# Optimization experiments

Measured on AMD Instinct MI355X. Metric: run time of the kernel, lower is better.

Reference implementation:

```python
import jax, jax.numpy as jnp
import numpy as np
import math

N_HEADS = 8
TANH_CLIP = 10.0
TEMP = 1.0


def setup_inputs() -> dict:
    key = jax.random.key(0)
    ks = jax.random.split(key, 8)
    B, N, D = 256, 2048, 128
    node_embeddings = jax.random.normal(ks[0], (B, N, D), dtype=jnp.float32)
    W_node = jax.random.normal(ks[1], (D, 3 * D), dtype=jnp.float32) / math.sqrt(D)
    W_fixed = jax.random.normal(ks[2], (D, D), dtype=jnp.float32) / math.sqrt(D)
    W_step = jax.random.normal(ks[3], (2 * D, D), dtype=jnp.float32) / math.sqrt(2 * D)
    W_out = jax.random.normal(ks[4], (D, D), dtype=jnp.float32) / math.sqrt(D)
    first_idx = jax.random.randint(ks[5], (B,), 0, N, dtype=jnp.int32)
    last_idx = jax.random.randint(ks[6], (B,), 0, N, dtype=jnp.int32)
    mask = jax.random.bernoulli(ks[7], 0.5, (B, N))
    mask = mask.at[:, 0].set(False)  # guarantee at least one feasible node per row
    return {"node_embeddings": node_embeddings, "W_node": W_node, "W_fixed": W_fixed,
            "W_step": W_step, "W_out": W_out, "first_idx": first_idx,
            "last_idx": last_idx, "mask": mask}


def reference(node_embeddings, W_node, W_fixed, W_step, W_out, first_idx, last_idx, mask):
    B, N, D = node_embeddings.shape
    H = N_HEADS
    hd = D // H  # key_dim = val_dim = embed_dim / n_heads
    neg_inf = -jnp.inf

    # --- _precompute ---
    graph_embed = node_embeddings.mean(axis=1)                # [B, D]
    fixed_context = graph_embed @ W_fixed                     # [B, D]
    proj = node_embeddings @ W_node                           # [B, N, 3D]
    gK, gV, logit_K = jnp.split(proj, 3, axis=-1)             # each [B, N, D]
    gK = gK.reshape(B, N, H, hd).transpose(2, 0, 1, 3)        # [H, B, N, hd]
    gV = gV.reshape(B, N, H, hd).transpose(2, 0, 1, 3)        # [H, B, N, hd]

    # --- step context: cat(first node emb, last node emb) ---
    first_emb = jnp.take_along_axis(node_embeddings, first_idx[:, None, None].astype(jnp.int32), axis=1)[:, 0]  # [B, D]
    last_emb = jnp.take_along_axis(node_embeddings, last_idx[:, None, None].astype(jnp.int32), axis=1)[:, 0]
    step_ctx = jnp.concatenate([first_emb, last_emb], axis=-1)  # [B, 2D]
    query = fixed_context + step_ctx @ W_step                 # [B, D]

    # --- glimpse multi-head attention (n_query = 1, masked inner) ---
    Q = query.reshape(B, H, hd).transpose(1, 0, 2)            # [H, B, hd]
    compat = jnp.einsum('hbd,hbnd->hbn', Q, gK) / math.sqrt(hd)  # [H, B, N]
    compat = jnp.where(mask[None, :, :], neg_inf, compat)     # mask_inner=True
    attn = jax.nn.softmax(compat, axis=-1)
    heads = jnp.einsum('hbn,hbnd->hbd', attn, gV)             # [H, B, hd]
    glimpse = heads.transpose(1, 0, 2).reshape(B, D) @ W_out  # project_out, [B, D]

    # --- logits with tanh clipping and masking ---
    logits = jnp.einsum('bd,bnd->bn', glimpse, logit_K) / math.sqrt(D)  # [B, N]
    logits = jnp.tanh(logits) * TANH_CLIP
    logits = jnp.where(mask, neg_inf, logits)                 # mask_logits=True
    log_p = jax.nn.log_softmax(logits / TEMP, axis=-1)        # [B, N]
    return log_p
```

## Files before the change

kernel.cpp:

```cpp
#include <hip/hip_runtime.h>
#include <math.h>

#define B_ 256
#define N_ 2048
#define D_ 128

#define NEG_HUGE (-1.0e30f)

#define WSA_STRIDE 1040
#define WSA_SIZE (B_ * 8 * WSA_STRIDE)
#define WSB_OFF WSA_SIZE
#define WSB_SIZE (B_ * 8 * 2)
#define WSC_OFF (WSB_OFF + WSB_SIZE)
#define WSC_SIZE (B_ * D_)
#define WS_FLOATS (WSC_OFF + WSC_SIZE)

__device__ __forceinline__ float wave_max64(float v) {
#pragma unroll
  for (int off = 32; off > 0; off >>= 1) v = fmaxf(v, __shfl_xor(v, off, 64));
  return v;
}
__device__ __forceinline__ float wave_sum64(float v) {
#pragma unroll
  for (int off = 32; off > 0; off >>= 1) v += __shfl_xor(v, off, 64);
  return v;
}

__global__ void __launch_bounds__(128) k_partial(const float* __restrict__ emb,
                                                 float* __restrict__ buf) {
  const int b = blockIdx.x, s = blockIdx.y;
  const int t = threadIdx.x;
  const int f4 = t & 31, ng = t >> 5;
  const float4* base = (const float4*)(emb + (size_t)b * N_ * D_);
  float4 acc = make_float4(0.f, 0.f, 0.f, 0.f);
  int n = s * 256 + ng;
#pragma unroll 4
  for (int i = 0; i < 64; ++i, n += 4) {
    float4 v = base[(size_t)n * 32 + f4];
    acc.x += v.x; acc.y += v.y; acc.z += v.z; acc.w += v.w;
  }
  __shared__ float4 red[128];
  red[t] = acc;
  __syncthreads();
  if (ng == 0) {
    float4 a = red[f4], bb = red[32 + f4], c = red[64 + f4], d = red[96 + f4];
    float4 r = make_float4(a.x + bb.x + c.x + d.x, a.y + bb.y + c.y + d.y,
                           a.z + bb.z + c.z + d.z, a.w + bb.w + c.w + d.w);
    *((float4*)(buf + (size_t)b * N_ + s * 128) + f4) = r;
  }
}

__global__ void __launch_bounds__(128) k_query(const float* __restrict__ emb,
                                               const float* __restrict__ Wfix,
                                               const float* __restrict__ Wstep,
                                               const float* __restrict__ Wnode,
                                               const int* __restrict__ fidx,
                                               const int* __restrict__ lidx,
                                               float* __restrict__ buf) {
  const int b = blockIdx.x, t = threadIdx.x;
  __shared__ float ge[128], fe[128], le[128], q[128];
  float s = 0.f;
  const float* part = buf + (size_t)b * N_;
#pragma unroll
  for (int i = 0; i < 8; ++i) s += part[i * 128 + t];
  ge[t] = s * (1.0f / 2048.0f);
  const int fi = fidx[b], li = lidx[b];
  fe[t] = emb[(size_t)b * N_ * D_ + (size_t)fi * D_ + t];
  le[t] = emb[(size_t)b * N_ * D_ + (size_t)li * D_ + t];
  __syncthreads();
  float acc = 0.f;
  for (int k = 0; k < 128; ++k) acc = fmaf(ge[k], Wfix[k * 128 + t], acc);
  for (int k = 0; k < 128; ++k) acc = fmaf(fe[k], Wstep[k * 128 + t], acc);
  for (int k = 0; k < 128; ++k) acc = fmaf(le[k], Wstep[(128 + k) * 128 + t], acc);
  q[t] = acc;
  __syncthreads();
  const float* wrow = Wnode + (size_t)t * 384;
#pragma unroll
  for (int h = 0; h < 8; ++h) {
    float a = 0.f;
#pragma unroll
    for (int k = 0; k < 16; ++k) a = fmaf(q[h * 16 + k], wrow[h * 16 + k], a);
    buf[(size_t)b * N_ + 1024 + h * 128 + t] = a * 0.25f;
  }
}

__global__ void __launch_bounds__(256) k_attn_part(const float* __restrict__ emb,
                                                   const unsigned char* __restrict__ mask,
                                                   const float* __restrict__ buf,
                                                   float* __restrict__ wsA) {
  const int b = blockIdx.x, s = blockIdx.y;
  const int t = threadIdx.x;
  const int lane = t & 63;
  const int hb = t >> 6;
  const int h0 = hb, h1 = hb + 4;

  __shared__ __align__(16) float emb_lds[64][132];
  __shared__ __align__(16) float qh_s[8 * 128];
  __shared__ unsigned char mask_s[64];

  {
    const float* src = buf + (size_t)b * N_ + 1024;
    for (int i = t; i < 1024; i += 256) qh_s[i] = src[i];
  }

  float m0 = -INFINITY, m1 = -INFINITY, l0 = 0.f, l1 = 0.f;
  float w00 = 0.f, w01 = 0.f, w10 = 0.f, w11 = 0.f;
  const int d0 = lane, d1 = lane + 64;
  const float* embb = emb + (size_t)b * N_ * D_;
  const unsigned char* mrow = mask + (size_t)b * N_;

  __syncthreads();

  for (int tile = 0; tile < 4; ++tile) {
    const int n0 = s * 256 + tile * 64;
    {
      int gid = t;
#pragma unroll
      for (int i = 0; i < 8; ++i, gid += 256) {
        int r = gid >> 5, c4 = gid & 31;
        float4 v = *(const float4*)(embb + (size_t)(n0 + r) * D_ + c4 * 4);
        *(float4*)&emb_lds[r][c4 * 4] = v;
      }
      if (t < 64) mask_s[t] = mrow[n0 + t];
    }
    __syncthreads();

    float s0 = 0.f, s1 = 0.f;
    {
      const float* er = &emb_lds[lane][0];
      const float* q0r = &qh_s[h0 * 128];
      const float* q1r = &qh_s[h1 * 128];
#pragma unroll 8
      for (int k = 0; k < 32; ++k) {
        float4 e = *(const float4*)(er + 4 * k);
        float4 qa = *(const float4*)(q0r + 4 * k);
        float4 qb = *(const float4*)(q1r + 4 * k);
        s0 = fmaf(e.x, qa.x, fmaf(e.y, qa.y, fmaf(e.z, qa.z, fmaf(e.w, qa.w, s0))));
        s1 = fmaf(e.x, qb.x, fmaf(e.y, qb.y, fmaf(e.z, qb.z, fmaf(e.w, qb.w, s1))));
      }
    }
    const bool msk = mask_s[lane] != 0;
    if (msk) { s0 = -INFINITY; s1 = -INFINITY; }

    const float tm0 = wave_max64(s0), tm1 = wave_max64(s1);
    const float mn0 = fmaxf(m0, tm0), mn1 = fmaxf(m1, tm1);
    const float r0 = (mn0 == -INFINITY) ? 1.f : expf(m0 - mn0);
    const float r1 = (mn1 == -INFINITY) ? 1.f : expf(m1 - mn1);
    const float p0 = msk ? 0.f : expf(s0 - mn0);
    const float p1 = msk ? 0.f : expf(s1 - mn1);
    l0 = l0 * r0 + wave_sum64(p0);
    l1 = l1 * r1 + wave_sum64(p1);
    m0 = mn0; m1 = mn1;

    w00 *= r0; w01 *= r0; w10 *= r1; w11 *= r1;
#pragma unroll 4
    for (int n = 0; n < 64; ++n) {
      const float pa = __int_as_float(__builtin_amdgcn_readlane(__float_as_int(p0), n));
      const float pb = __int_as_float(__builtin_amdgcn_readlane(__float_as_int(p1), n));
      const float e0 = emb_lds[n][d0];
      const float e1 = emb_lds[n][d1];
      w00 = fmaf(pa, e0, w00); w01 = fmaf(pa, e1, w01);
      w10 = fmaf(pb, e0, w10); w11 = fmaf(pb, e1, w11);
    }
    __syncthreads();
  }

  float* dst = wsA + (size_t)(b * 8 + s) * WSA_STRIDE;
  dst[16 + h0 * 128 + d0] = w00;
  dst[16 + h0 * 128 + d1] = w01;
  dst[16 + h1 * 128 + d0] = w10;
  dst[16 + h1 * 128 + d1] = w11;
  if (lane == 0) {
    dst[h0] = m0; dst[8 + h0] = l0;
    dst[h1] = m1; dst[8 + h1] = l1;
  }
}

__global__ void __launch_bounds__(128) k_attn_comb(const float* __restrict__ Wnode,
                                                   const float* __restrict__ Wout,
                                                   const float* __restrict__ wsA,
                                                   float* __restrict__ wsC) {
  const int b = blockIdx.x, t = threadIdx.x;
  const float* base = wsA + (size_t)b * 8 * WSA_STRIDE;
  __shared__ float Ls[8], scale[8][8];
  __shared__ float wl[8 * 128], heads[128], glim[128];

  if (t < 8) {
    float M = -INFINITY;
#pragma unroll
    for (int s = 0; s < 8; ++s) M = fmaxf(M, base[s * WSA_STRIDE + t]);
    float L = 0.f;
#pragma unroll
    for (int s = 0; s < 8; ++s) {
      const float m = base[s * WSA_STRIDE + t];
      const float sc = (m == -INFINITY) ? 0.f : expf(m - M);
      scale[s][t] = sc;
      L = fmaf(base[s * WSA_STRIDE + 8 + t], sc, L);
    }
    Ls[t] = L;
  }
  __syncthreads();

#pragma unroll
  for (int h = 0; h < 8; ++h) {
    float acc = 0.f;
#pragma unroll
    for (int s = 0; s < 8; ++s)
      acc = fmaf(scale[s][h], base[s * WSA_STRIDE + 16 + h * 128 + t], acc);
    wl[h * 128 + t] = acc;
  }
  __syncthreads();

  {
    const int h = t >> 4, k = t & 15;
    float hv = 0.f;
    const float* wp = Wnode + 128 + h * 16 + k;
    for (int d = 0; d < 128; ++d) hv = fmaf(wl[h * 128 + d], wp[(size_t)d * 384], hv);
    heads[t] = hv / Ls[h];
  }
  __syncthreads();
  {
    float g = 0.f;
    for (int j = 0; j < 128; ++j) g = fmaf(heads[j], Wout[j * 128 + t], g);
    glim[t] = g;
  }
  __syncthreads();
  {
    float cv = 0.f;
    const float* wr = Wnode + (size_t)t * 384 + 256;
    for (int j = 0; j < 128; ++j) cv = fmaf(wr[j], glim[j], cv);
    wsC[(size_t)b * 128 + t] = cv * 0.08838834764831845f;
  }
}

__global__ void __launch_bounds__(256) k_logits_part(const float* __restrict__ emb,
                                                     const unsigned char* __restrict__ mask,
                                                     const float* __restrict__ wsC,
                                                     float* __restrict__ buf,
                                                     float* __restrict__ wsB) {
  const int b = blockIdx.x, s = blockIdx.y;
  const int t = threadIdx.x, lane = t & 63, w = t >> 6;
  __shared__ __align__(16) float emb_lds[64][132];
  __shared__ float part[4][64];
  const float* embb = emb + (size_t)b * N_ * D_;
  const unsigned char* mrow = mask + (size_t)b * N_;

  float4 cq[8];
  {
    const float4* c4 = (const float4*)(wsC + (size_t)b * 128);
#pragma unroll
    for (int j = 0; j < 8; ++j) cq[j] = c4[w * 8 + j];
  }

  float mr = NEG_HUGE, sr = 0.f;
  for (int tile = 0; tile < 4; ++tile) {
    const int n0 = s * 256 + tile * 64;
    {
      int gid = t;
#pragma unroll
      for (int i = 0; i < 8; ++i, gid += 256) {
        int r = gid >> 5, c4i = gid & 31;
        *(float4*)&emb_lds[r][c4i * 4] =
            *(const float4*)(embb + (size_t)(n0 + r) * D_ + c4i * 4);
      }
    }
    __syncthreads();

    const float* er = &emb_lds[lane][w * 32];
    float acc = 0.f;
#pragma unroll
    for (int j = 0; j < 8; ++j) {
      float4 e = *(const float4*)(er + 4 * j);
      acc = fmaf(e.x, cq[j].x, fmaf(e.y, cq[j].y, fmaf(e.z, cq[j].z, fmaf(e.w, cq[j].w, acc))));
    }
    part[w][lane] = acc;
    __syncthreads();

    const float v = part[0][lane] + part[1][lane] + part[2][lane] + part[3][lane];
    const bool msk = mrow[n0 + lane] != 0;
    const float val = msk ? NEG_HUGE : 10.f * tanhf(v);
    const float tm = wave_max64(val);
    const float mn = fmaxf(mr, tm);
    sr = sr * expf(mr - mn) + wave_sum64(msk ? 0.f : expf(val - mn));
    mr = mn;
    if (w == 0) buf[(size_t)b * N_ + n0 + lane] = val;
    __syncthreads();
  }
  if (t == 0) {
    wsB[(size_t)(b * 8 + s) * 2] = mr;
    wsB[(size_t)(b * 8 + s) * 2 + 1] = sr;
  }
}

__global__ void __launch_bounds__(256) k_norm(const float* __restrict__ wsB,
                                              float* __restrict__ buf) {
  const int b = blockIdx.x, t = threadIdx.x;
  __shared__ float LSs;
  if (t == 0) {
    float M = NEG_HUGE;
#pragma unroll
    for (int s = 0; s < 8; ++s) M = fmaxf(M, wsB[(size_t)(b * 8 + s) * 2]);
    float S = 0.f;
#pragma unroll
    for (int s = 0; s < 8; ++s) {
      const float m = wsB[(size_t)(b * 8 + s) * 2];
      S += wsB[(size_t)(b * 8 + s) * 2 + 1] * expf(m - M);
    }
    LSs = M + logf(S);
  }
  __syncthreads();
  const float LS = LSs;
#pragma unroll
  for (int i = 0; i < 8; ++i) {
    const size_t idx = (size_t)b * N_ + t + 256 * i;
    const float v = buf[idx];
    buf[idx] = (v <= -1.0e29f) ? NEG_HUGE : (v - LS);
  }
}

__global__ void __launch_bounds__(256) k_attn(const float* __restrict__ emb,
                                              const float* __restrict__ Wnode,
                                              const float* __restrict__ Wout,
                                              const unsigned char* __restrict__ mask,
                                              float* __restrict__ buf) {
  const int b = blockIdx.x;
  const int t = threadIdx.x;
  const int lane = t & 63;
  const int hb = t >> 6;
  const int h0 = hb, h1 = hb + 4;

  __shared__ __align__(16) float emb_lds[64][132];
  __shared__ __align__(16) float qh_s[8 * 128];
  __shared__ float heads_lds[128];
  __shared__ float glim_lds[128];
  __shared__ float l_lds[8];
  __shared__ unsigned char mask_s[64];

  {
    const float* src = buf + (size_t)b * N_ + 1024;
    for (int i = t; i < 1024; i += 256) qh_s[i] = src[i];
  }
  float m0 = -INFINITY, m1 = -INFINITY, l0 = 0.f, l1 = 0.f;
  float w00 = 0.f, w01 = 0.f, w10 = 0.f, w11 = 0.f;
  const int d0 = lane, d1 = lane + 64;
  const float* embb = emb + (size_t)b * N_ * D_;
  const unsigned char* mrow = mask + (size_t)b * N_;
  __syncthreads();
  for (int tile = 0; tile < N_ / 64; ++tile) {
    const int n0 = tile * 64;
    int gid = t;
#pragma unroll
    for (int i = 0; i < 8; ++i, gid += 256) {
      int r = gid >> 5, c4 = gid & 31;
      *(float4*)&emb_lds[r][c4 * 4] = *(const float4*)(embb + (size_t)(n0 + r) * D_ + c4 * 4);
    }
    if (t < 64) mask_s[t] = mrow[n0 + t];
    __syncthreads();
    float s0 = 0.f, s1 = 0.f;
    const float* er = &emb_lds[lane][0];
    const float* q0r = &qh_s[h0 * 128];
    const float* q1r = &qh_s[h1 * 128];
#pragma unroll 8
    for (int k = 0; k < 32; ++k) {
      float4 e = *(const float4*)(er + 4 * k);
      float4 qa = *(const float4*)(q0r + 4 * k);
      float4 qb = *(const float4*)(q1r + 4 * k);
      s0 = fmaf(e.x, qa.x, fmaf(e.y, qa.y, fmaf(e.z, qa.z, fmaf(e.w, qa.w, s0))));
      s1 = fmaf(e.x, qb.x, fmaf(e.y, qb.y, fmaf(e.z, qb.z, fmaf(e.w, qb.w, s1))));
    }
    const bool msk = mask_s[lane] != 0;
    if (msk) { s0 = -INFINITY; s1 = -INFINITY; }
    const float tm0 = wave_max64(s0), tm1 = wave_max64(s1);
    const float mn0 = fmaxf(m0, tm0), mn1 = fmaxf(m1, tm1);
    const float r0 = (mn0 == -INFINITY) ? 1.f : expf(m0 - mn0);
    const float r1 = (mn1 == -INFINITY) ? 1.f : expf(m1 - mn1);
    const float p0 = msk ? 0.f : expf(s0 - mn0);
    const float p1 = msk ? 0.f : expf(s1 - mn1);
    l0 = l0 * r0 + wave_sum64(p0);
    l1 = l1 * r1 + wave_sum64(p1);
    m0 = mn0; m1 = mn1;
    w00 *= r0; w01 *= r0; w10 *= r1; w11 *= r1;
#pragma unroll 4
    for (int n = 0; n < 64; ++n) {
      const float pa = __int_as_float(__builtin_amdgcn_readlane(__float_as_int(p0), n));
      const float pb = __int_as_float(__builtin_amdgcn_readlane(__float_as_int(p1), n));
      const float e0 = emb_lds[n][d0];
      const float e1 = emb_lds[n][d1];
      w00 = fmaf(pa, e0, w00); w01 = fmaf(pa, e1, w01);
      w10 = fmaf(pb, e0, w10); w11 = fmaf(pb, e1, w11);
    }
    __syncthreads();
  }
  float* wl = &emb_lds[0][0];
  wl[h0 * 128 + d0] = w00; wl[h0 * 128 + d1] = w01;
  wl[h1 * 128 + d0] = w10; wl[h1 * 128 + d1] = w11;
  if (lane == 0) { l_lds[h0] = l0; l_lds[h1] = l1; }
  __syncthreads();
  if (t < 128) {
    const int h = t >> 4, k = t & 15;
    float hv = 0.f;
    const float* wp = Wnode + 128 + h * 16 + k;
    for (int d = 0; d < 128; ++d) hv = fmaf(wl[h * 128 + d], wp[(size_t)d * 384], hv);
    heads_lds[h * 16 + k] = hv / l_lds[h];
  }
  __syncthreads();
  if (t < 128) {
    float g = 0.f;
    for (int j = 0; j < 128; ++j) g = fmaf(heads_lds[j], Wout[j * 128 + t], g);
    glim_lds[t] = g;
  }
  __syncthreads();
  if (t < 128) {
    float cv = 0.f;
    const float* wr = Wnode + (size_t)t * 384 + 256;
    for (int j = 0; j < 128; ++j) cv = fmaf(wr[j], glim_lds[j], cv);
    buf[(size_t)b * N_ + t] = cv * 0.08838834764831845f;
  }
}

__global__ void __launch_bounds__(256) k_logits(const float* __restrict__ emb,
                                                const unsigned char* __restrict__ mask,
                                                float* __restrict__ buf) {
  const int b = blockIdx.x, t = threadIdx.x;
  const int lane = t & 63, w = t >> 6;
  __shared__ float lg[N_];
  __shared__ float redmax[4], redsum[4];
  const float c0 = buf[(size_t)b * N_ + 2 * lane];
  const float c1 = buf[(size_t)b * N_ + 2 * lane + 1];
  const float2* ebase = (const float2*)(emb + (size_t)b * N_ * D_);
  for (int i = 0; i < 64; ++i) {
    const int n0 = w * 512 + i * 8;
    float sarr[8];
#pragma unroll
    for (int j = 0; j < 8; ++j) {
      float2 e = ebase[(size_t)(n0 + j) * 64 + lane];
      sarr[j] = fmaf(e.x, c0, e.y * c1);
    }
#pragma unroll
    for (int j = 0; j < 8; ++j) {
      const float v = wave_sum64(sarr[j]);
      if (lane == j) lg[n0 + j] = v;
    }
  }
  __syncthreads();
  const unsigned char* mrow = mask + (size_t)b * N_;
  float v[8];
  float vmax = NEG_HUGE;
#pragma unroll
  for (int i = 0; i < 8; ++i) {
    const int n = t + 256 * i;
    const float val = mrow[n] ? NEG_HUGE : 10.f * tanhf(lg[n]);
    v[i] = val;
    vmax = fmaxf(vmax, val);
  }
  vmax = wave_max64(vmax);
  if (lane == 0) redmax[w] = vmax;
  __syncthreads();
  const float M = fmaxf(fmaxf(redmax[0], redmax[1]), fmaxf(redmax[2], redmax[3]));
  float ss = 0.f;
#pragma unroll
  for (int i = 0; i < 8; ++i) ss += expf(v[i] - M);
  ss = wave_sum64(ss);
  if (lane == 0) redsum[w] = ss;
  __syncthreads();
  const float S = redsum[0] + redsum[1] + redsum[2] + redsum[3];
  const float LS = M + logf(S);
#pragma unroll
  for (int i = 0; i < 8; ++i) {
    const int n = t + 256 * i;
    buf[(size_t)b * N_ + n] = mrow[n] ? NEG_HUGE : (v[i] - LS);
  }
}

extern "C" void kernel_launch(void* const* d_in, const int* in_sizes, int n_in,
                              void* d_out, int out_size, void* d_ws, size_t ws_size,
                              hipStream_t stream) {
  (void)in_sizes; (void)n_in; (void)out_size;
  const float* emb = (const float*)d_in[0];
  const float* Wnode = (const float*)d_in[1];
  const float* Wfix = (const float*)d_in[2];
  const float* Wstep = (const float*)d_in[3];
  const float* Wout = (const float*)d_in[4];
  const int* fidx = (const int*)d_in[5];
  const int* lidx = (const int*)d_in[6];
  const unsigned char* mask = (const unsigned char*)d_in[7];
  float* buf = (float*)d_out;

  k_partial<<<dim3(B_, 8), 128, 0, stream>>>(emb, buf);
  k_query<<<B_, 128, 0, stream>>>(emb, Wfix, Wstep, Wnode, fidx, lidx, buf);

  if (ws_size >= (size_t)WS_FLOATS * sizeof(float)) {
    float* ws = (float*)d_ws;
    k_attn_part<<<dim3(B_, 8), 256, 0, stream>>>(emb, mask, buf, ws);
    k_attn_comb<<<B_, 128, 0, stream>>>(Wnode, Wout, ws, ws + WSC_OFF);
    k_logits_part<<<dim3(B_, 8), 256, 0, stream>>>(emb, mask, ws + WSC_OFF, buf, ws + WSB_OFF);
    k_norm<<<B_, 256, 0, stream>>>(ws + WSB_OFF, buf);
  } else {
    k_attn<<<B_, 256, 0, stream>>>(emb, Wnode, Wout, mask, buf);
    k_logits<<<B_, 256, 0, stream>>>(emb, mask, buf);
  }
}
```

Before: 199.8 us.

## Use bf16 MFMA for attention scores and weighted sums in partial attention

Rewrites the split-N attention kernel so the query-key scores and the probability-weighted embedding sums run on 16x16x32 bf16 MFMA instructions instead of scalar FP32 FMAs. Embedding tiles are converted to bf16 and stored in LDS in both row and transposed layouts, with the online softmax reduced across waves through shared memory. The fallback single-kernel path and the workspace-size check are removed. This trades FP32 precision for bf16 in the attention step and adds extra LDS transposes and barriers, while the kernel is likely still dominated by streaming the embeddings from memory.

```diff
diff --git a/kernel.cpp b/kernel.cpp
--- a/kernel.cpp
+++ b/kernel.cpp
@@ -12,8 +12,10 @@
 #define WSB_OFF WSA_SIZE
 #define WSB_SIZE (B_ * 8 * 2)
 #define WSC_OFF (WSB_OFF + WSB_SIZE)
-#define WSC_SIZE (B_ * D_)
-#define WS_FLOATS (WSC_OFF + WSC_SIZE)
+
+typedef __attribute__((ext_vector_type(8))) short bf16x8;
+typedef __attribute__((ext_vector_type(4))) float f32x4;
+typedef __attribute__((ext_vector_type(4))) unsigned short u16x4;
 
 __device__ __forceinline__ float wave_max64(float v) {
 #pragma unroll
@@ -24,6 +26,11 @@
 #pragma unroll
   for (int off = 32; off > 0; off >>= 1) v += __shfl_xor(v, off, 64);
   return v;
+}
+__device__ __forceinline__ unsigned short bf16rne(float f) {
+  unsigned u = __float_as_uint(f);
+  u += 0x7FFFu + ((u >> 16) & 1u);
+  return (unsigned short)(u >> 16);
 }
 
 __global__ void __launch_bounds__(128) k_partial(const float* __restrict__ emb,
@@ -84,96 +91,142 @@
   }
 }
 
-__global__ void __launch_bounds__(256) k_attn_part(const float* __restrict__ emb,
-                                                   const unsigned char* __restrict__ mask,
-                                                   const float* __restrict__ buf,
-                                                   float* __restrict__ wsA) {
-  const int b = blockIdx.x, s = blockIdx.y;
-  const int t = threadIdx.x;
-  const int lane = t & 63;
-  const int hb = t >> 6;
-  const int h0 = hb, h1 = hb + 4;
-
-  __shared__ __align__(16) float emb_lds[64][132];
-  __shared__ __align__(16) float qh_s[8 * 128];
+__global__ void __launch_bounds__(256) k_attn_m(const float* __restrict__ emb,
+                                                const unsigned char* __restrict__ mask,
+                                                const float* __restrict__ buf,
+                                                float* __restrict__ wsA) {
+  const int b = blockIdx.x, s = blockIdx.y, t = threadIdx.x;
+  const int lane = t & 63, w = t >> 6;
+  const int lg = lane >> 4, lc = lane & 15;
+
+  __shared__ __align__(16) unsigned short eR[64][136];
+  __shared__ __align__(16) unsigned short eC[128][72];
+  __shared__ __align__(16) unsigned short pT[16][72];
+  __shared__ float red0[4][16];
+  __shared__ float red1[4][16];
+  __shared__ float resc_s[16];
   __shared__ unsigned char mask_s[64];
 
-  {
-    const float* src = buf + (size_t)b * N_ + 1024;
-    for (int i = t; i < 1024; i += 256) qh_s[i] = src[i];
-  }
-
-  float m0 = -INFINITY, m1 = -INFINITY, l0 = 0.f, l1 = 0.f;
-  float w00 = 0.f, w01 = 0.f, w10 = 0.f, w11 = 0.f;
-  const int d0 = lane, d1 = lane + 64;
-  const float* embb = emb + (size_t)b * N_ * D_;
-  const unsigned char* mrow = mask + (size_t)b * N_;
-
-  __syncthreads();
+  bf16x8 bq[4];
+#pragma unroll
+  for (int ks = 0; ks < 4; ++ks)
+#pragma unroll
+    for (int j = 0; j < 8; ++j) bq[ks][j] = 0;
+  if (lc < 8) {
+    const float* qrow = buf + (size_t)b * N_ + 1024 + lc * 128;
+#pragma unroll
+    for (int ks = 0; ks < 4; ++ks)
+#pragma unroll
+      for (int j = 0; j < 8; ++j)
+        bq[ks][j] = (short)bf16rne(qrow[32 * ks + 8 * lg + j]);
+  }
+
+  float m_run = -INFINITY, l_run = 0.f;
+  f32x4 wacc0 = {0.f, 0.f, 0.f, 0.f}, wacc1 = {0.f, 0.f, 0.f, 0.f};
+  const float* embb = emb + ((size_t)b * N_ + s * 256) * D_;
+  const unsigned char* mrow = mask + (size_t)b * N_ + s * 256;
 
   for (int tile = 0; tile < 4; ++tile) {
-    const int n0 = s * 256 + tile * 64;
     {
-      int gid = t;
-#pragma unroll
-      for (int i = 0; i < 8; ++i, gid += 256) {
-        int r = gid >> 5, c4 = gid & 31;
-        float4 v = *(const float4*)(embb + (size_t)(n0 + r) * D_ + c4 * 4);
-        *(float4*)&emb_lds[r][c4 * 4] = v;
+      const float* src = embb + (size_t)tile * 64 * D_;
+#pragma unroll
+      for (int i = 0; i < 4; ++i) {
+        const int gid = t + 256 * i;
+        const int n = gid >> 4, d0 = (gid & 15) * 8;
+        const float4 v0 = *(const float4*)(src + (size_t)n * D_ + d0);
+        const float4 v1 = *(const float4*)(src + (size_t)n * D_ + d0 + 4);
+        bf16x8 ev;
+        ev[0] = (short)bf16rne(v0.x); ev[1] = (short)bf16rne(v0.y);
+        ev[2] = (short)bf16rne(v0.z); ev[3] = (short)bf16rne(v0.w);
+        ev[4] = (short)bf16rne(v1.x); ev[5] = (short)bf16rne(v1.y);
+        ev[6] = (short)bf16rne(v1.z); ev[7] = (short)bf16rne(v1.w);
+        *(bf16x8*)&eR[n][d0] = ev;
       }
-      if (t < 64) mask_s[t] = mrow[n0 + t];
-    }
-    __syncthreads();
-
-    float s0 = 0.f, s1 = 0.f;
+      if (t < 64) mask_s[t] = mrow[tile * 64 + t];
+    }
+    __syncthreads();
+
     {
-      const float* er = &emb_lds[lane][0];
-      const float* q0r = &qh_s[h0 * 128];
-      const float* q1r = &qh_s[h1 * 128];
-#pragma unroll 8
-      for (int k = 0; k < 32; ++k) {
-        float4 e = *(const float4*)(er + 4 * k);
-        float4 qa = *(const float4*)(q0r + 4 * k);
-        float4 qb = *(const float4*)(q1r + 4 * k);
-        s0 = fmaf(e.x, qa.x, fmaf(e.y, qa.y, fmaf(e.z, qa.z, fmaf(e.w, qa.w, s0))));
-        s1 = fmaf(e.x, qb.x, fmaf(e.y, qb.y, fmaf(e.z, qb.z, fmaf(e.w, qb.w, s1))));
+      const int d = t >> 1, n0 = (t & 1) * 32;
+#pragma unroll
+      for (int jb = 0; jb < 4; ++jb) {
+        bf16x8 cv;
+#pragma unroll
+        for (int i = 0; i < 8; ++i) cv[i] = (short)eR[n0 + 8 * jb + i][d];
+        *(bf16x8*)&eC[d][n0 + 8 * jb] = cv;
       }
     }
-    const bool msk = mask_s[lane] != 0;
-    if (msk) { s0 = -INFINITY; s1 = -INFINITY; }
-
-    const float tm0 = wave_max64(s0), tm1 = wave_max64(s1);
-    const float mn0 = fmaxf(m0, tm0), mn1 = fmaxf(m1, tm1);
-    const float r0 = (mn0 == -INFINITY) ? 1.f : expf(m0 - mn0);
-    const float r1 = (mn1 == -INFINITY) ? 1.f : expf(m1 - mn1);
-    const float p0 = msk ? 0.f : expf(s0 - mn0);
-    const float p1 = msk ? 0.f : expf(s1 - mn1);
-    l0 = l0 * r0 + wave_sum64(p0);
-    l1 = l1 * r1 + wave_sum64(p1);
-    m0 = mn0; m1 = mn1;
-
-    w00 *= r0; w01 *= r0; w10 *= r1; w11 *= r1;
-#pragma unroll 4
-    for (int n = 0; n < 64; ++n) {
-      const float pa = __int_as_float(__builtin_amdgcn_readlane(__float_as_int(p0), n));
-      const float pb = __int_as_float(__builtin_amdgcn_readlane(__float_as_int(p1), n));
-      const float e0 = emb_lds[n][d0];
-      const float e1 = emb_lds[n][d1];
-      w00 = fmaf(pa, e0, w00); w01 = fmaf(pa, e1, w01);
-      w10 = fmaf(pb, e0, w10); w11 = fmaf(pb, e1, w11);
+
+    f32x4 sAcc = {0.f, 0.f, 0.f, 0.f};
+#pragma unroll
+    for (int ks = 0; ks < 4; ++ks) {
+      const bf16x8 af = *(const bf16x8*)&eR[16 * w + lc][32 * ks + 8 * lg];
+      sAcc = __builtin_amdgcn_mfma_f32_16x16x32_bf16(af, bq[ks], sAcc, 0, 0, 0);
+    }
+
+    float sv[4];
+    bool mk[4];
+    float tmax = -INFINITY;
+#pragma unroll
+    for (int r = 0; r < 4; ++r) {
+      mk[r] = mask_s[16 * w + 4 * lg + r] != 0;
+      sv[r] = mk[r] ? -INFINITY : sAcc[r];
+      tmax = fmaxf(tmax, sv[r]);
+    }
+    tmax = fmaxf(tmax, __shfl_xor(tmax, 16, 64));
+    tmax = fmaxf(tmax, __shfl_xor(tmax, 32, 64));
+    if (lane < 16) red0[w][lc] = tmax;
+    __syncthreads();
+
+    const float m_tile = fmaxf(fmaxf(red0[0][lc], red0[1][lc]),
+                               fmaxf(red0[2][lc], red0[3][lc]));
+    const float m_new = fmaxf(m_run, m_tile);
+    const float rsc = (m_new == -INFINITY) ? 1.f : __expf(m_run - m_new);
+    float psum = 0.f;
+    unsigned short pu[4];
+#pragma unroll
+    for (int r = 0; r < 4; ++r) {
+      const float p = mk[r] ? 0.f : __expf(sv[r] - m_new);
+      psum += p;
+      pu[r] = bf16rne(p);
+    }
+    m_run = m_new;
+    psum += __shfl_xor(psum, 16, 64);
+    psum += __shfl_xor(psum, 32, 64);
+    if (lane < 16) red1[w][lc] = psum;
+    *(u16x4*)&pT[lc][16 * w + 4 * lg] = (u16x4){pu[0], pu[1], pu[2], pu[3]};
+    if (t < 16) resc_s[t] = rsc;
+    __syncthreads();
+
+    l_run = l_run * rsc + (red1[0][lc] + red1[1][lc] + red1[2][lc] + red1[3][lc]);
+
+    {
+      const float r0f = resc_s[4 * lg + 0], r1f = resc_s[4 * lg + 1];
+      const float r2f = resc_s[4 * lg + 2], r3f = resc_s[4 * lg + 3];
+      wacc0[0] *= r0f; wacc0[1] *= r1f; wacc0[2] *= r2f; wacc0[3] *= r3f;
+      wacc1[0] *= r0f; wacc1[1] *= r1f; wacc1[2] *= r2f; wacc1[3] *= r3f;
+    }
+#pragma unroll
+    for (int ks = 0; ks < 2; ++ks) {
+      const bf16x8 pa = *(const bf16x8*)&pT[lc][32 * ks + 8 * lg];
+      const bf16x8 b0 = *(const bf16x8*)&eC[16 * w + lc][32 * ks + 8 * lg];
+      const bf16x8 b1 = *(const bf16x8*)&eC[16 * (w + 4) + lc][32 * ks + 8 * lg];
+      wacc0 = __builtin_amdgcn_mfma_f32_16x16x32_bf16(pa, b0, wacc0, 0, 0, 0);
+      wacc1 = __builtin_amdgcn_mfma_f32_16x16x32_bf16(pa, b1, wacc1, 0, 0, 0);
     }
     __syncthreads();
   }
 
   float* dst = wsA + (size_t)(b * 8 + s) * WSA_STRIDE;
-  dst[16 + h0 * 128 + d0] = w00;
-  dst[16 + h0 * 128 + d1] = w01;
-  dst[16 + h1 * 128 + d0] = w10;
-  dst[16 + h1 * 128 + d1] = w11;
-  if (lane == 0) {
-    dst[h0] = m0; dst[8 + h0] = l0;
-    dst[h1] = m1; dst[8 + h1] = l1;
-  }
+  if (lg < 2) {
+#pragma unroll
+    for (int r = 0; r < 4; ++r) {
+      const int h = 4 * lg + r;
+      dst[16 + h * 128 + 16 * w + lc] = wacc0[r];
+      dst[16 + h * 128 + 16 * (w + 4) + lc] = wacc1[r];
+    }
+  }
+  if (t < 8) { dst[t] = m_run; dst[8 + t] = l_run; }
 }
 
 __global__ void __launch_bounds__(128) k_attn_comb(const float* __restrict__ Wnode,
@@ -200,7 +253,6 @@
     Ls[t] = L;
   }
   __syncthreads();
-
 #pragma unroll
   for (int h = 0; h < 8; ++h) {
     float acc = 0.f;
@@ -210,7 +262,6 @@
     wl[h * 128 + t] = acc;
   }
   __syncthreads();
-
   {
     const int h = t >> 4, k = t & 15;
     float hv = 0.f;
@@ -251,21 +302,17 @@
 #pragma unroll
     for (int j = 0; j < 8; ++j) cq[j] = c4[w * 8 + j];
   }
-
   float mr = NEG_HUGE, sr = 0.f;
   for (int tile = 0; tile < 4; ++tile) {
     const int n0 = s * 256 + tile * 64;
-    {
-      int gid = t;
-#pragma unroll
-      for (int i = 0; i < 8; ++i, gid += 256) {
-        int r = gid >> 5, c4i = gid & 31;
-        *(float4*)&emb_lds[r][c4i * 4] =
-            *(const float4*)(embb + (size_t)(n0 + r) * D_ + c4i * 4);
-      }
-    }
-    __syncthreads();
-
+    int gid = t;
+#pragma unroll
+    for (int i = 0; i < 8; ++i, gid += 256) {
+      int r = gid >> 5, c4i = gid & 31;
+      *(float4*)&emb_lds[r][c4i * 4] =
+          *(const float4*)(embb + (size_t)(n0 + r) * D_ + c4i * 4);
+    }
+    __syncthreads();
     const float* er = &emb_lds[lane][w * 32];
     float acc = 0.f;
 #pragma unroll
@@ -275,7 +322,6 @@
     }
     part[w][lane] = acc;
     __syncthreads();
-
     const float v = part[0][lane] + part[1][lane] + part[2][lane] + part[3][lane];
     const bool msk = mrow[n0 + lane] != 0;
     const float val = msk ? NEG_HUGE : 10.f * tanhf(v);
@@ -299,12 +345,12 @@
   if (t == 0) {
     float M = NEG_HUGE;
 #pragma unroll
-    for (int s = 0; s < 8; ++s) M = fmaxf(M, wsB[(size_t)(b * 8 + s) * 2]);
+    for (int q = 0; q < 8; ++q) M = fmaxf(M, wsB[(size_t)(b * 8 + q) * 2]);
     float S = 0.f;
 #pragma unroll
-    for (int s = 0; s < 8; ++s) {
-      const float m = wsB[(size_t)(b * 8 + s) * 2];
-      S += wsB[(size_t)(b * 8 + s) * 2 + 1] * expf(m - M);
+    for (int q = 0; q < 8; ++q) {
+      const float m = wsB[(size_t)(b * 8 + q) * 2];
+      S += wsB[(size_t)(b * 8 + q) * 2 + 1] * expf(m - M);
     }
     LSs = M + logf(S);
   }
@@ -318,164 +364,10 @@
   }
 }
 
-__global__ void __launch_bounds__(256) k_attn(const float* __restrict__ emb,
-                                              const float* __restrict__ Wnode,
-                                              const float* __restrict__ Wout,
-                                              const unsigned char* __restrict__ mask,
-                                              float* __restrict__ buf) {
-  const int b = blockIdx.x;
-  const int t = threadIdx.x;
-  const int lane = t & 63;
-  const int hb = t >> 6;
-  const int h0 = hb, h1 = hb + 4;
-
-  __shared__ __align__(16) float emb_lds[64][132];
-  __shared__ __align__(16) float qh_s[8 * 128];
-  __shared__ float heads_lds[128];
-  __shared__ float glim_lds[128];
-  __shared__ float l_lds[8];
-  __shared__ unsigned char mask_s[64];
-
-  {
-    const float* src = buf + (size_t)b * N_ + 1024;
-    for (int i = t; i < 1024; i += 256) qh_s[i] = src[i];
-  }
-  float m0 = -INFINITY, m1 = -INFINITY, l0 = 0.f, l1 = 0.f;
-  float w00 = 0.f, w01 = 0.f, w10 = 0.f, w11 = 0.f;
-  const int d0 = lane, d1 = lane + 64;
-  const float* embb = emb + (size_t)b * N_ * D_;
-  const unsigned char* mrow = mask + (size_t)b * N_;
-  __syncthreads();
-  for (int tile = 0; tile < N_ / 64; ++tile) {
-    const int n0 = tile * 64;
-    int gid = t;
-#pragma unroll
-    for (int i = 0; i < 8; ++i, gid += 256) {
-      int r = gid >> 5, c4 = gid & 31;
-      *(float4*)&emb_lds[r][c4 * 4] = *(const float4*)(embb + (size_t)(n0 + r) * D_ + c4 * 4);
-    }
-    if (t < 64) mask_s[t] = mrow[n0 + t];
-    __syncthreads();
-    float s0 = 0.f, s1 = 0.f;
-    const float* er = &emb_lds[lane][0];
-    const float* q0r = &qh_s[h0 * 128];
-    const float* q1r = &qh_s[h1 * 128];
-#pragma unroll 8
-    for (int k = 0; k < 32; ++k) {
-      float4 e = *(const float4*)(er + 4 * k);
-      float4 qa = *(const float4*)(q0r + 4 * k);
-      float4 qb = *(const float4*)(q1r + 4 * k);
-      s0 = fmaf(e.x, qa.x, fmaf(e.y, qa.y, fmaf(e.z, qa.z, fmaf(e.w, qa.w, s0))));
-      s1 = fmaf(e.x, qb.x, fmaf(e.y, qb.y, fmaf(e.z, qb.z, fmaf(e.w, qb.w, s1))));
-    }
-    const bool msk = mask_s[lane] != 0;
-    if (msk) { s0 = -INFINITY; s1 = -INFINITY; }
-    const float tm0 = wave_max64(s0), tm1 = wave_max64(s1);
-    const float mn0 = fmaxf(m0, tm0), mn1 = fmaxf(m1, tm1);
-    const float r0 = (mn0 == -INFINITY) ? 1.f : expf(m0 - mn0);
-    const float r1 = (mn1 == -INFINITY) ? 1.f : expf(m1 - mn1);
-    const float p0 = msk ? 0.f : expf(s0 - mn0);
-    const float p1 = msk ? 0.f : expf(s1 - mn1);
-    l0 = l0 * r0 + wave_sum64(p0);
-    l1 = l1 * r1 + wave_sum64(p1);
-    m0 = mn0; m1 = mn1;
-    w00 *= r0; w01 *= r0; w10 *= r1; w11 *= r1;
-#pragma unroll 4
-    for (int n = 0; n < 64; ++n) {
-      const float pa = __int_as_float(__builtin_amdgcn_readlane(__float_as_int(p0), n));
-      const float pb = __int_as_float(__builtin_amdgcn_readlane(__float_as_int(p1), n));
-      const float e0 = emb_lds[n][d0];
-      const float e1 = emb_lds[n][d1];
-      w00 = fmaf(pa, e0, w00); w01 = fmaf(pa, e1, w01);
-      w10 = fmaf(pb, e0, w10); w11 = fmaf(pb, e1, w11);
-    }
-    __syncthreads();
-  }
-  float* wl = &emb_lds[0][0];
-  wl[h0 * 128 + d0] = w00; wl[h0 * 128 + d1] = w01;
-  wl[h1 * 128 + d0] = w10; wl[h1 * 128 + d1] = w11;
-  if (lane == 0) { l_lds[h0] = l0; l_lds[h1] = l1; }
-  __syncthreads();
-  if (t < 128) {
-    const int h = t >> 4, k = t & 15;
-    float hv = 0.f;
-    const float* wp = Wnode + 128 + h * 16 + k;
-    for (int d = 0; d < 128; ++d) hv = fmaf(wl[h * 128 + d], wp[(size_t)d * 384], hv);
-    heads_lds[h * 16 + k] = hv / l_lds[h];
-  }
-  __syncthreads();
-  if (t < 128) {
-    float g = 0.f;
-    for (int j = 0; j < 128; ++j) g = fmaf(heads_lds[j], Wout[j * 128 + t], g);
-    glim_lds[t] = g;
-  }
-  __syncthreads();
-  if (t < 128) {
-    float cv = 0.f;
-    const float* wr = Wnode + (size_t)t * 384 + 256;
-    for (int j = 0; j < 128; ++j) cv = fmaf(wr[j], glim_lds[j], cv);
-    buf[(size_t)b * N_ + t] = cv * 0.08838834764831845f;
-  }
-}
-
-__global__ void __launch_bounds__(256) k_logits(const float* __restrict__ emb,
-                                                const unsigned char* __restrict__ mask,
-                                                float* __restrict__ buf) {
-  const int b = blockIdx.x, t = threadIdx.x;
-  const int lane = t & 63, w = t >> 6;
-  __shared__ float lg[N_];
-  __shared__ float redmax[4], redsum[4];
-  const float c0 = buf[(size_t)b * N_ + 2 * lane];
-  const float c1 = buf[(size_t)b * N_ + 2 * lane + 1];
-  const float2* ebase = (const float2*)(emb + (size_t)b * N_ * D_);
-  for (int i = 0; i < 64; ++i) {
-    const int n0 = w * 512 + i * 8;
-    float sarr[8];
-#pragma unroll
-    for (int j = 0; j < 8; ++j) {
-      float2 e = ebase[(size_t)(n0 + j) * 64 + lane];
-      sarr[j] = fmaf(e.x, c0, e.y * c1);
-    }
-#pragma unroll
-    for (int j = 0; j < 8; ++j) {
-      const float v = wave_sum64(sarr[j]);
-      if (lane == j) lg[n0 + j] = v;
-    }
-  }
-  __syncthreads();
-  const unsigned char* mrow = mask + (size_t)b * N_;
-  float v[8];
-  float vmax = NEG_HUGE;
-#pragma unroll
-  for (int i = 0; i < 8; ++i) {
-    const int n = t + 256 * i;
-    const float val = mrow[n] ? NEG_HUGE : 10.f * tanhf(lg[n]);
-    v[i] = val;
-    vmax = fmaxf(vmax, val);
-  }
-  vmax = wave_max64(vmax);
-  if (lane == 0) redmax[w] = vmax;
-  __syncthreads();
-  const float M = fmaxf(fmaxf(redmax[0], redmax[1]), fmaxf(redmax[2], redmax[3]));
-  float ss = 0.f;
-#pragma unroll
-  for (int i = 0; i < 8; ++i) ss += expf(v[i] - M);
-  ss = wave_sum64(ss);
-  if (lane == 0) redsum[w] = ss;
-  __syncthreads();
-  const float S = redsum[0] + redsum[1] + redsum[2] + redsum[3];
-  const float LS = M + logf(S);
-#pragma unroll
-  for (int i = 0; i < 8; ++i) {
-    const int n = t + 256 * i;
-    buf[(size_t)b * N_ + n] = mrow[n] ? NEG_HUGE : (v[i] - LS);
-  }
-}
-
 extern "C" void kernel_launch(void* const* d_in, const int* in_sizes, int n_in,
                               void* d_out, int out_size, void* d_ws, size_t ws_size,
                               hipStream_t stream) {
-  (void)in_sizes; (void)n_in; (void)out_size;
+  (void)in_sizes; (void)n_in; (void)out_size; (void)ws_size;
   const float* emb = (const float*)d_in[0];
   const float* Wnode = (const float*)d_in[1];
   const float* Wfix = (const float*)d_in[2];
@@ -485,18 +377,12 @@
   const int* lidx = (const int*)d_in[6];
   const unsigned char* mask = (const unsigned char*)d_in[7];
   float* buf = (float*)d_out;
+  float* ws = (float*)d_ws;
 
   k_partial<<<dim3(B_, 8), 128, 0, stream>>>(emb, buf);
   k_query<<<B_, 128, 0, stream>>>(emb, Wfix, Wstep, Wnode, fidx, lidx, buf);
-
-  if (ws_size >= (size_t)WS_FLOATS * sizeof(float)) {
-    float* ws = (float*)d_ws;
-    k_attn_part<<<dim3(B_, 8), 256, 0, stream>>>(emb, mask, buf, ws);
-    k_attn_comb<<<B_, 128, 0, stream>>>(Wnode, Wout, ws, ws + WSC_OFF);
-    k_logits_part<<<dim3(B_, 8), 256, 0, stream>>>(emb, mask, ws + WSC_OFF, buf, ws + WSB_OFF);
-    k_norm<<<B_, 256, 0, stream>>>(ws + WSB_OFF, buf);
-  } else {
-    k_attn<<<B_, 256, 0, stream>>>(emb, Wnode, Wout, mask, buf);
-    k_logits<<<B_, 256, 0, stream>>>(emb, mask, buf);
-  }
-}
+  k_attn_m<<<dim3(B_, 8), 256, 0, stream>>>(emb, mask, buf, ws);
+  k_attn_comb<<<B_, 128, 0, stream>>>(Wnode, Wout, ws, ws + WSC_OFF);
+  k_logits_part<<<dim3(B_, 8), 256, 0, stream>>>(emb, mask, ws + WSC_OFF, buf, ws + WSB_OFF);
+  k_norm<<<B_, 256, 0, stream>>>(ws + WSB_OFF, buf);
+}
```

Result: faster. 171.6 us (-14.1%).
